# Optimization experiments

Hardware: AMD Instinct MI355X
Metric: run time of the kernel (lower is better)

The kernel has to match this reference:

```python
import jax, jax.numpy as jnp
import numpy as np

L = 16          # num_slices
RMIN, RMAX = 0.4, 0.9
B_, C_, H_, W_, N_ = 2, 4, 64, 64, 64   # n = 64 scan steps, last dim of x = N_*L


def setup_inputs() -> dict:
    key = jax.random.key(0)
    k = jax.random.split(key, 8)
    u1 = jax.random.uniform(k[0], (L,), dtype=jnp.float32)
    u2 = jax.random.uniform(k[1], (L,), dtype=jnp.float32)
    theta = 2.0 * np.pi * u2
    nu_log = jnp.log(-0.5 * jnp.log(u1 * (RMAX ** 2 - RMIN ** 2) + RMIN ** 2))
    # torch.complex(exp(-exp(nu_log)), theta): real part = modulus-like term, imag = theta
    Lambda_re = jnp.exp(-jnp.exp(nu_log))
    Lambda_im = theta
    B_re = jax.random.normal(k[2], (L, L), dtype=jnp.float32)
    B_im = jax.random.normal(k[3], (L, L), dtype=jnp.float32)
    C_re = jax.random.normal(k[4], (L, L), dtype=jnp.float32)
    C_im = jax.random.normal(k[5], (L, L), dtype=jnp.float32)
    D = jax.random.normal(k[6], (L, L), dtype=jnp.float32)
    x = jax.random.normal(k[7], (B_, C_, H_, W_, N_ * L), dtype=jnp.float32)
    return {"x": x, "Lambda_re": Lambda_re, "Lambda_im": Lambda_im,
            "B_re": B_re, "B_im": B_im, "C_re": C_re, "C_im": C_im, "D": D}


def reference(x, Lambda_re, Lambda_im, B_re, B_im, C_re, C_im, D):
    l = Lambda_re.shape[0]
    b, c, h, w, nl = x.shape
    n = nl // l
    img = x.reshape(b, c, h, w, n, l)                       # 'b c h w (n l) -> b c h w n l'
    Lam = jax.lax.complex(Lambda_re, Lambda_im)             # (l,) complex64
    Bc = jax.lax.complex(B_re, B_im)                        # (l,l) complex64
    Cc = jax.lax.complex(C_re, C_im)
    out = img.astype(jnp.complex64)
    # Faithful Hillis-Steele loop with op(x, y) = Lambda*x + B @ y
    for d in range(1, int(np.log2(n)) + 1):
        step = 2 ** (d - 1)
        left = out[..., : n - step, :]
        right = out[..., step:, :]
        new = left * Lam + jnp.einsum('kl,bchwnl->bchwnk', Bc, right)
        out = jnp.concatenate([out[..., :step, :], new], axis=-2)
    y = jnp.real(jnp.einsum('kl,bchwnl->bchwnk', Cc, out)) \
        + jnp.einsum('kl,bchwnl->bchwnk', D, img)
    return y
```

## Files before the change

### kernel.cpp

```cpp
#include <hip/hip_runtime.h>
#include <hip/hip_bf16.h>


namespace {

typedef __attribute__((ext_vector_type(8))) short short8v;
typedef __attribute__((ext_vector_type(4))) float f32x4;
typedef __attribute__((ext_vector_type(4))) unsigned uint4v;

__device__ inline unsigned short f2bf_rne(float f) {
    unsigned u = __builtin_bit_cast(unsigned, f);
    u += 0x7fffu + ((u >> 16) & 1u);
    return (unsigned short)(u >> 16);
}

__device__ inline void gld_lds16(const unsigned short* g, unsigned short* l) {
    __builtin_amdgcn_global_load_lds(
        (const __attribute__((address_space(1))) unsigned int*)g,
        (__attribute__((address_space(3))) unsigned int*)l, 16, 0, 0);
}

__device__ inline unsigned pk2(float a, float b) {
    __hip_bfloat162 h = __float22bfloat162_rn(make_float2(a, b));
    unsigned r;
    __builtin_memcpy(&r, &h, 4);
    return r;
}


__global__ __launch_bounds__(256) void build_w_kernel(
    const float* __restrict__ Lre, const float* __restrict__ Lim,
    const float* __restrict__ Bre, const float* __restrict__ Bim,
    const float* __restrict__ Cre, const float* __restrict__ Cim,
    const float* __restrict__ Dm,
    unsigned short* __restrict__ Wh)
{
    const int i = blockIdx.x >> 6, j = blockIdx.x & 63;
    const int t = threadIdx.x, k = t >> 4, l = t & 15;

    const int n_g = i * 16 + k;
    const int k_g = j * 16 + l;
    const size_t widx = (((size_t)((n_g >> 7) * 32 + (k_g >> 5))) << 12)
                      + (((k_g >> 3) & 3) << 10) + ((n_g & 127) << 3) + (k_g & 7);

    if (j > i) { Wh[widx] = 0; return; }

    __shared__ float2 Bs[16][16];
    __shared__ float2 M[16][16];
    Bs[k][l] = make_float2(Bre[t], Bim[t]);
    M[k][l]  = make_float2(k == l ? 1.f : 0.f, 0.f);
    const int delta = i - j;
    __syncthreads();

    #pragma unroll
    for (int d = 0; d < 6; ++d) {
        const int s = 1 << d;
        if (delta & s) {
            const float lr = Lre[k], li = Lim[k];
            const float2 m0 = M[k][l];
            M[k][l] = make_float2(lr * m0.x - li * m0.y, lr * m0.y + li * m0.x);
            __syncthreads();
        } else if (j + (delta & (s - 1)) >= s) {
            float2 acc = make_float2(0.f, 0.f);
            #pragma unroll
            for (int m = 0; m < 16; ++m) {
                const float2 b = Bs[k][m], v = M[m][l];
                acc.x += b.x * v.x - b.y * v.y;
                acc.y += b.x * v.y + b.y * v.x;
            }
            __syncthreads();
            M[k][l] = acc;
            __syncthreads();
        }
    }

    float w = 0.f;
    #pragma unroll
    for (int m = 0; m < 16; ++m) {
        const float2 v = M[m][l];
        w += Cre[k * 16 + m] * v.x - Cim[k * 16 + m] * v.y;
    }
    if (i == j) w += Dm[t];
    Wh[widx] = f2bf_rne(w);
}

__global__ __launch_bounds__(256) void gemm_fused_kernel(
    const float* __restrict__ X,
    const unsigned short* __restrict__ Wh,
    float* __restrict__ Y, int mtiles)
{
    __shared__ alignas(16) float sA[2][4096];
    __shared__ alignas(16) unsigned short sB[2][4096];

    const int bid = blockIdx.x;
    const int nb = 7 - bid / mtiles;
    const int mt = bid % mtiles;
    const int t = threadIdx.x;
    const int wid = t >> 6, lane = t & 63;
    const int wr = wid >> 1, wc = wid & 1;
    const int l15 = lane & 15, lg = lane >> 4;
    const int nt = (nb + 1) * 4;

    f32x4 acc[4][4] = {};

    int arow[4], as0[4], as1[4];
    #pragma unroll
    for (int mm = 0; mm < 4; ++mm) {
        const int row = wr * 64 + mm * 16 + l15;
        arow[mm] = row << 5;
        as0[mm] = (((2 * lg)     ^ (row & 7)) << 2);
        as1[mm] = (((2 * lg + 1) ^ (row & 7)) << 2);
    }
    int bfo[4];
    #pragma unroll
    for (int nn = 0; nn < 4; ++nn)
        bfo[nn] = (lg << 10) + ((wc * 64 + nn * 16 + l15) << 3);

    auto stageT = [&](int b, int tk) {
        float* bA = sA[b];
        unsigned short* bB = sB[b];
        const float* xbase = X + (size_t)mt * 131072 + tk * 32;
        #pragma unroll
        for (int p = 0; p < 4; ++p) {
            const int s = p * 256 + t;
            const int row = s >> 3, kq = s & 7;
            const float* src = xbase + (size_t)row * 1024 + ((kq ^ (row & 7)) << 2);
            gld_lds16((const unsigned short*)src, (unsigned short*)(bA + s * 4));
        }
        const unsigned short* wb = Wh + (((size_t)(nb * 32 + tk)) << 12);
        #pragma unroll
        for (int p = 0; p < 2; ++p) {
            const int e8 = (p * 256 + t) * 8;
            gld_lds16(wb + e8, bB + e8);
        }
    };

    stageT(0, 0);
    __syncthreads();

    for (int tk = 0; tk < nt; ++tk) {
        const int c = tk & 1;
        if (tk + 1 < nt) stageT(c ^ 1, tk + 1);

        short8v ah[4];
        #pragma unroll
        for (int mm = 0; mm < 4; ++mm) {
            const f32x4 q0 = *reinterpret_cast<const f32x4*>(sA[c] + arow[mm] + as0[mm]);
            const f32x4 q1 = *reinterpret_cast<const f32x4*>(sA[c] + arow[mm] + as1[mm]);
            uint4v uv;
            uv[0] = pk2(q0[0], q0[1]);
            uv[1] = pk2(q0[2], q0[3]);
            uv[2] = pk2(q1[0], q1[1]);
            uv[3] = pk2(q1[2], q1[3]);
            short8v r;
            __builtin_memcpy(&r, &uv, 16);
            ah[mm] = r;
        }
        short8v bh[4];
        #pragma unroll
        for (int nn = 0; nn < 4; ++nn)
            bh[nn] = *reinterpret_cast<const short8v*>(sB[c] + bfo[nn]);

        __builtin_amdgcn_s_setprio(1);
        #pragma unroll
        for (int mm = 0; mm < 4; ++mm)
            #pragma unroll
            for (int nn = 0; nn < 4; ++nn)
                acc[mm][nn] = __builtin_amdgcn_mfma_f32_16x16x32_bf16(
                    ah[mm], bh[nn], acc[mm][nn], 0, 0, 0);
        __builtin_amdgcn_s_setprio(0);

        __syncthreads();
    }

    #pragma unroll
    for (int mm = 0; mm < 4; ++mm) {
        const int grow = mt * 128 + wr * 64 + mm * 16 + lg * 4;
        #pragma unroll
        for (int nn = 0; nn < 4; ++nn) {
            const int gcol = nb * 128 + wc * 64 + nn * 16 + l15;
            #pragma unroll
            for (int q = 0; q < 4; ++q)
                Y[(size_t)(grow + q) * 1024 + gcol] = acc[mm][nn][q];
        }
    }
}

}

extern "C" void kernel_launch(void* const* d_in, const int* in_sizes, int n_in,
                              void* d_out, int out_size, void* d_ws, size_t ws_size,
                              hipStream_t stream) {
    const float* x   = (const float*)d_in[0];
    const float* Lre = (const float*)d_in[1];
    const float* Lim = (const float*)d_in[2];
    const float* Bre = (const float*)d_in[3];
    const float* Bim = (const float*)d_in[4];
    const float* Cre = (const float*)d_in[5];
    const float* Cim = (const float*)d_in[6];
    const float* Dm  = (const float*)d_in[7];
    float* y = (float*)d_out;

    const int positions = in_sizes[0] / 1024;
    const int mtiles = positions / 128;

    unsigned short* Wh = (unsigned short*)d_ws;

    build_w_kernel<<<4096, 256, 0, stream>>>(Lre, Lim, Bre, Bim, Cre, Cim, Dm, Wh);
    gemm_fused_kernel<<<mtiles * 8, 256, 0, stream>>>(x, Wh, y, mtiles);
}
```

Measured before the change: 98.76 us.

## Convert X to bf16 once at staging via register prefetch, explicit pipeline

X tiles are now loaded into registers two steps ahead, converted to bf16, and stored into LDS in the same K-major fragment layout as W. Previously fp32 was copied to LDS and each wave repacked it before every MFMA. This halves LDS footprint and traffic for A and removes redundant per-wave conversion. The cost is hand-managed waitcnt/barrier scheduling and more registers, and the vmcnt counts must stay exactly right.

```diff
diff --git a/kernel.cpp b/kernel.cpp
--- a/kernel.cpp
+++ b/kernel.cpp
@@ -6,7 +6,6 @@
 
 typedef __attribute__((ext_vector_type(8))) short short8v;
 typedef __attribute__((ext_vector_type(4))) float f32x4;
-typedef __attribute__((ext_vector_type(4))) unsigned uint4v;
 
 __device__ inline unsigned short f2bf_rne(float f) {
     unsigned u = __builtin_bit_cast(unsigned, f);
@@ -89,7 +88,7 @@
     const unsigned short* __restrict__ Wh,
     float* __restrict__ Y, int mtiles)
 {
-    __shared__ alignas(16) float sA[2][4096];
+    __shared__ alignas(16) unsigned short sA[2][4096];
     __shared__ alignas(16) unsigned short sB[2][4096];
 
     const int bid = blockIdx.x;
@@ -103,64 +102,54 @@
 
     f32x4 acc[4][4] = {};
 
-    int arow[4], as0[4], as1[4];
-    #pragma unroll
-    for (int mm = 0; mm < 4; ++mm) {
-        const int row = wr * 64 + mm * 16 + l15;
-        arow[mm] = row << 5;
-        as0[mm] = (((2 * lg)     ^ (row & 7)) << 2);
-        as1[mm] = (((2 * lg + 1) ^ (row & 7)) << 2);
-    }
-    int bfo[4];
+    int afo[4], bfo[4];
+    #pragma unroll
+    for (int mm = 0; mm < 4; ++mm)
+        afo[mm] = (lg << 10) + ((wr * 64 + mm * 16 + l15) << 3);
     #pragma unroll
     for (int nn = 0; nn < 4; ++nn)
         bfo[nn] = (lg << 10) + ((wc * 64 + nn * 16 + l15) << 3);
 
-    auto stageT = [&](int b, int tk) {
-        float* bA = sA[b];
-        unsigned short* bB = sB[b];
-        const float* xbase = X + (size_t)mt * 131072 + tk * 32;
-        #pragma unroll
-        for (int p = 0; p < 4; ++p) {
-            const int s = p * 256 + t;
-            const int row = s >> 3, kq = s & 7;
-            const float* src = xbase + (size_t)row * 1024 + ((kq ^ (row & 7)) << 2);
-            gld_lds16((const unsigned short*)src, (unsigned short*)(bA + s * 4));
-        }
+    const int row0 = t >> 2, kq = t & 3;
+    const float* xr0 = X + (size_t)(mt * 128 + row0) * 1024 + kq * 8;
+    const float* xr1 = xr0 + (size_t)64 * 1024;
+    const int aw0 = (kq << 10) + (row0 << 3);
+    const int aw1 = (kq << 10) + ((row0 + 64) << 3);
+
+    float4 ar0[4], ar1[4];
+
+    auto issueA = [&](float4* ar, int tk) {
+        const float* s0 = xr0 + tk * 32;
+        const float* s1 = xr1 + tk * 32;
+        ar[0] = *reinterpret_cast<const float4*>(s0);
+        ar[1] = *reinterpret_cast<const float4*>(s0 + 4);
+        ar[2] = *reinterpret_cast<const float4*>(s1);
+        ar[3] = *reinterpret_cast<const float4*>(s1 + 4);
+    };
+    auto writeA = [&](unsigned short* bufA, const float4* ar) {
+        short8v v0, v1;
+        unsigned u0[4] = { pk2(ar[0].x, ar[0].y), pk2(ar[0].z, ar[0].w),
+                           pk2(ar[1].x, ar[1].y), pk2(ar[1].z, ar[1].w) };
+        unsigned u1[4] = { pk2(ar[2].x, ar[2].y), pk2(ar[2].z, ar[2].w),
+                           pk2(ar[3].x, ar[3].y), pk2(ar[3].z, ar[3].w) };
+        __builtin_memcpy(&v0, u0, 16);
+        __builtin_memcpy(&v1, u1, 16);
+        *reinterpret_cast<short8v*>(bufA + aw0) = v0;
+        *reinterpret_cast<short8v*>(bufA + aw1) = v1;
+    };
+    auto stageW = [&](unsigned short* bufB, int tk) {
         const unsigned short* wb = Wh + (((size_t)(nb * 32 + tk)) << 12);
-        #pragma unroll
-        for (int p = 0; p < 2; ++p) {
-            const int e8 = (p * 256 + t) * 8;
-            gld_lds16(wb + e8, bB + e8);
-        }
-    };
-
-    stageT(0, 0);
-    __syncthreads();
-
-    for (int tk = 0; tk < nt; ++tk) {
-        const int c = tk & 1;
-        if (tk + 1 < nt) stageT(c ^ 1, tk + 1);
-
-        short8v ah[4];
-        #pragma unroll
-        for (int mm = 0; mm < 4; ++mm) {
-            const f32x4 q0 = *reinterpret_cast<const f32x4*>(sA[c] + arow[mm] + as0[mm]);
-            const f32x4 q1 = *reinterpret_cast<const f32x4*>(sA[c] + arow[mm] + as1[mm]);
-            uint4v uv;
-            uv[0] = pk2(q0[0], q0[1]);
-            uv[1] = pk2(q0[2], q0[3]);
-            uv[2] = pk2(q1[0], q1[1]);
-            uv[3] = pk2(q1[2], q1[3]);
-            short8v r;
-            __builtin_memcpy(&r, &uv, 16);
-            ah[mm] = r;
-        }
-        short8v bh[4];
+        gld_lds16(wb + t * 8,        bufB + t * 8);
+        gld_lds16(wb + 2048 + t * 8, bufB + 2048 + t * 8);
+    };
+    auto compute = [&](const unsigned short* bufA, const unsigned short* bufB) {
+        short8v ah[4], bh[4];
+        #pragma unroll
+        for (int mm = 0; mm < 4; ++mm)
+            ah[mm] = *reinterpret_cast<const short8v*>(bufA + afo[mm]);
         #pragma unroll
         for (int nn = 0; nn < 4; ++nn)
-            bh[nn] = *reinterpret_cast<const short8v*>(sB[c] + bfo[nn]);
-
+            bh[nn] = *reinterpret_cast<const short8v*>(bufB + bfo[nn]);
         __builtin_amdgcn_s_setprio(1);
         #pragma unroll
         for (int mm = 0; mm < 4; ++mm)
@@ -169,8 +158,54 @@
                 acc[mm][nn] = __builtin_amdgcn_mfma_f32_16x16x32_bf16(
                     ah[mm], bh[nn], acc[mm][nn], 0, 0, 0);
         __builtin_amdgcn_s_setprio(0);
-
-        __syncthreads();
+    };
+
+    issueA(ar0, 0);
+    stageW(sB[0], 0);
+    issueA(ar1, 1);
+    asm volatile("s_waitcnt vmcnt(4)" ::: "memory");
+    __builtin_amdgcn_sched_barrier(0);
+    writeA(sA[0], ar0);
+    asm volatile("s_waitcnt lgkmcnt(0)" ::: "memory");
+    __builtin_amdgcn_s_barrier();
+    __builtin_amdgcn_sched_barrier(0);
+
+    for (int tk = 0; tk < nt; tk += 2) {
+        stageW(sB[1], tk + 1);
+        __builtin_amdgcn_sched_barrier(0);
+        if (tk + 2 < nt) issueA(ar0, tk + 2);
+        __builtin_amdgcn_sched_barrier(0);
+        compute(sA[0], sB[0]);
+        if (tk + 2 < nt) {
+            asm volatile("s_waitcnt vmcnt(4)" ::: "memory");
+        } else {
+            asm volatile("s_waitcnt vmcnt(0)" ::: "memory");
+        }
+        __builtin_amdgcn_sched_barrier(0);
+        writeA(sA[1], ar1);
+        asm volatile("s_waitcnt lgkmcnt(0)" ::: "memory");
+        __builtin_amdgcn_s_barrier();
+        __builtin_amdgcn_sched_barrier(0);
+
+        if (tk + 2 < nt) {
+            stageW(sB[0], tk + 2);
+            __builtin_amdgcn_sched_barrier(0);
+            if (tk + 3 < nt) issueA(ar1, tk + 3);
+            __builtin_amdgcn_sched_barrier(0);
+        }
+        compute(sA[1], sB[1]);
+        if (tk + 2 < nt) {
+            if (tk + 3 < nt) {
+                asm volatile("s_waitcnt vmcnt(4)" ::: "memory");
+            } else {
+                asm volatile("s_waitcnt vmcnt(0)" ::: "memory");
+            }
+            __builtin_amdgcn_sched_barrier(0);
+            writeA(sA[0], ar0);
+            asm volatile("s_waitcnt lgkmcnt(0)" ::: "memory");
+            __builtin_amdgcn_s_barrier();
+            __builtin_amdgcn_sched_barrier(0);
+        }
     }
 
     #pragma unroll
```

New measurement: 112.5 us. +13.9%, slower.
